# Performance work log

Hardware: AMD Instinct MI355X
Metric: run time of the kernel (lower is better)

Reference implementation:

```python
import jax, jax.numpy as jnp
import numpy as np

THETA = 10000.0

def apply_rope(x, positions):
    # x: [B, H, S, d_k], positions: [S] int
    d_k = x.shape[-1]
    inv_freq = THETA ** (-jnp.arange(0, d_k, 2, dtype=jnp.float32) / d_k)  # [d_k/2]
    ang = positions.astype(jnp.float32)[:, None] * inv_freq[None, :]        # [S, d_k/2]
    cos, sin = jnp.cos(ang), jnp.sin(ang)
    x_even = x[..., 0::2]
    x_odd = x[..., 1::2]
    r_even = x_even * cos - x_odd * sin
    r_odd = x_even * sin + x_odd * cos
    # interleave back
    return jnp.stack([r_even, r_odd], axis=-1).reshape(x.shape)

def setup_inputs() -> dict:
    key = jax.random.key(0)
    k1, k2, k3 = jax.random.split(key, 3)
    B, S, D = 2, 2048, 1024
    x = jax.random.normal(k1, (B, S, D), dtype=jnp.float32)
    token_positions = jnp.arange(S, dtype=jnp.int32)
    W_qkv = jax.random.normal(k2, (3 * D, D), dtype=jnp.float32) * 0.02
    W_o = jax.random.normal(k3, (D, D), dtype=jnp.float32) * 0.02
    return {"x": x, "token_positions": token_positions, "W_qkv": W_qkv, "W_o": W_o}

def reference(x, token_positions, W_qkv, W_o):
    B, S, D = x.shape
    H = 16
    d_k = D // H
    qkv = jnp.einsum('bsd,ed->bse', x, W_qkv)           # [B, S, 3D]
    q, k, v = jnp.split(qkv, 3, axis=-1)
    def to_heads(t):
        return t.reshape(B, S, H, d_k).transpose(0, 2, 1, 3)  # [B, H, S, d_k]
    hq, hk, hv = to_heads(q), to_heads(k), to_heads(v)
    hq = apply_rope(hq, token_positions)
    hk = apply_rope(hk, token_positions)
    scale = d_k ** -0.5
    scores = jnp.einsum('bhqd,bhkd->bhqk', hq, hk) * scale  # [B, H, S, S]
    causal = jnp.tril(jnp.ones((S, S), dtype=bool))
    scores = jnp.where(causal, scores, -jnp.inf)
    attn = jax.nn.softmax(scores, axis=-1)
    out = jnp.einsum('bhqk,bhkd->bhqd', attn, hv)           # [B, H, S, d_k]
    out = out.transpose(0, 2, 1, 3).reshape(B, S, D)
    return jnp.einsum('bsd,ed->bse', out, W_o)
```

## Files before the change

kernel.cpp:

```cpp
#include <hip/hip_runtime.h>
#include <math.h>

typedef short short8 __attribute__((ext_vector_type(8)));
typedef float f32x4 __attribute__((ext_vector_type(4)));

typedef __attribute__((address_space(1))) const void* as1p;
typedef __attribute__((address_space(3))) void* as3p;

__device__ __forceinline__ unsigned short f2bf(float f) {
    unsigned int u = __float_as_uint(f);
    u += 0x7fffu + ((u >> 16) & 1u);
    return (unsigned short)(u >> 16);
}
__device__ __forceinline__ float bf2f(unsigned int bits) {
    return __uint_as_float(bits << 16);
}

__global__ void cvt_all_bf16(const float* __restrict__ x,
                             const float* __restrict__ wqkv,
                             const float* __restrict__ wo,
                             unsigned short* __restrict__ xb,
                             unsigned short* __restrict__ wqkvb,
                             unsigned short* __restrict__ wob) {
    int i = blockIdx.x * blockDim.x + threadIdx.x;
    const float* src;
    unsigned short* dst;
    int off;
    if (i < 1048576)       { src = x;    dst = xb;    off = i; }
    else if (i < 1835008)  { src = wqkv; dst = wqkvb; off = i - 1048576; }
    else                   { src = wo;   dst = wob;   off = i - 1835008; }
    float4 v = ((const float4*)src)[off];
    ushort4 o = make_ushort4(f2bf(v.x), f2bf(v.y), f2bf(v.z), f2bf(v.w));
    ((ushort4*)dst)[off] = o;
}

template <int RF, int NTX, bool BF16_OUT, bool DO_ROPE>
__global__ __launch_bounds__(256) void gemm_nt_mfma(
    const unsigned short* __restrict__ A, const unsigned short* __restrict__ B,
    void* __restrict__ Cv, const int* __restrict__ pos, int N, int K) {
    constexpr int BM = RF * 32;
    __shared__ unsigned short As[BM * 32];
    __shared__ unsigned short Bs[128 * 32];
    const int tid = threadIdx.x;
    const int wave = tid >> 6, lane = tid & 63;
    const int L = blockIdx.x;
    const int xcd = L & 7, idx = L >> 3;
    const int nt_ = xcd * NTX + idx % NTX;
    const int mt  = idx / NTX;
    const int m0 = mt * BM, n0 = nt_ << 7;
    const int wr = ((wave >> 1) & 1) * (RF * 16);
    const int wc = (wave & 1) << 6;

    const int r0 = tid >> 2;
    const int ko = (((tid & 3) ^ ((r0 >> 1) & 3)) << 3);
    const unsigned short* Ap0 = A + (size_t)(m0 + r0) * K + ko;
    const unsigned short* Ap1 = A + (size_t)(m0 + (RF == 4 ? 64 : 0) + r0) * K + ko;
    const unsigned short* Bp0 = B + (size_t)(n0 + r0) * K + ko;
    const unsigned short* Bp1 = B + (size_t)(n0 + 64 + r0) * K + ko;

    f32x4 acc[RF][4] = {};
    const int lro = lane & 15;
    const int cs = ((lane >> 4) ^ ((lro >> 1) & 3)) << 3;

    for (int k0 = 0; k0 < K; k0 += 32) {
        __syncthreads();
        __builtin_amdgcn_global_load_lds((as1p)(Ap0 + k0), (as3p)(As + tid * 8), 16, 0, 0);
        if constexpr (RF == 4)
            __builtin_amdgcn_global_load_lds((as1p)(Ap1 + k0), (as3p)(As + (256 + tid) * 8), 16, 0, 0);
        __builtin_amdgcn_global_load_lds((as1p)(Bp0 + k0), (as3p)(Bs + tid * 8), 16, 0, 0);
        __builtin_amdgcn_global_load_lds((as1p)(Bp1 + k0), (as3p)(Bs + (256 + tid) * 8), 16, 0, 0);
        __syncthreads();

        short8 af[RF], bfr[4];
        #pragma unroll
        for (int i = 0; i < RF; i++) af[i] = *(const short8*)&As[(wr + i * 16 + lro) * 32 + cs];
        #pragma unroll
        for (int j = 0; j < 4; j++) bfr[j] = *(const short8*)&Bs[(wc + j * 16 + lro) * 32 + cs];
        #pragma unroll
        for (int i = 0; i < RF; i++)
            #pragma unroll
            for (int j = 0; j < 4; j++)
                acc[i][j] = __builtin_amdgcn_mfma_f32_16x16x32_bf16(af[i], bfr[j], acc[i][j], 0, 0, 0);
    }

    const int row_b = m0 + wr + ((lane >> 4) << 2);
    const int col_b = n0 + wc + lro;

    if constexpr (DO_ROPE) {
        const int sec = (n0 + wc) >> 10;
        if (sec < 2) {
            const float qs = (sec == 0) ? 0.18033688011112042f : 1.0f;
            const float sgn = (lane & 1) ? 1.0f : -1.0f;
            float ps[RF * 4];
            #pragma unroll
            for (int i = 0; i < RF; i++)
                #pragma unroll
                for (int r = 0; r < 4; r++)
                    ps[i * 4 + r] = (float)pos[(row_b + i * 16 + r) & 2047];
            #pragma unroll
            for (int j = 0; j < 4; j++) {
                float invf_rev = exp2f(-(float)((lro >> 1) + 8 * j) * 0.41524101186092029f)
                                 * 0.15915494309189535f;
                #pragma unroll
                for (int i = 0; i < RF; i++)
                    #pragma unroll
                    for (int r = 0; r < 4; r++) {
                        float rev = ps[i * 4 + r] * invf_rev;
                        rev -= floorf(rev);
                        float c = __builtin_amdgcn_cosf(rev) * qs;
                        float s = __builtin_amdgcn_sinf(rev) * (qs * sgn);
                        float mine = acc[i][j][r];
                        float partner = __shfl_xor(mine, 1, 64);
                        acc[i][j][r] = mine * c + partner * s;
                    }
            }
        }
    }

    #pragma unroll
    for (int i = 0; i < RF; i++)
        #pragma unroll
        for (int j = 0; j < 4; j++)
            #pragma unroll
            for (int r = 0; r < 4; r++) {
                size_t idx2 = (size_t)(row_b + i * 16 + r) * N + (col_b + j * 16);
                if constexpr (BF16_OUT) ((unsigned short*)Cv)[idx2] = f2bf(acc[i][j][r]);
                else ((float*)Cv)[idx2] = acc[i][j][r];
            }
}

__global__ __launch_bounds__(256) void flash_attn_mfma(
    const unsigned short* __restrict__ qkv, unsigned short* __restrict__ Ows) {
    const int S = 2048, D3 = 3072;
    const int L = blockIdx.x;
    const int xcd = L & 7, rr = L >> 3;
    const int qt = 31 - (rr >> 2);
    const int g2 = xcd + ((rr & 3) << 3);
    const int h = g2 & 15, b = g2 >> 4;
    const int tid = threadIdx.x, wave = tid >> 6, lane = tid & 63;
    const int lro = lane & 15, grp = lane >> 4;

    __shared__ __align__(16) unsigned short Ks[2][64 * 64];
    __shared__ __align__(16) unsigned int   Vp[2][64 * 36];
    __shared__ __align__(16) unsigned short Ps[64 * 80];

    const int sr = tid >> 3;
    const int sc = ((tid & 7) ^ (sr & 7)) << 3;
    const int kp = tid >> 3, vo = (tid & 7) << 3;
    const int vka = (kp >> 1) + ((kp & 1) << 5);
    const int vcol = (((kp >> 2) ^ (tid & 7)) << 2) | (kp & 3);

    const int cq = grp ^ (lro & 7);
    int kof0[4], kof1[4], vbse[4], vq[4];
    #pragma unroll
    for (int nt = 0; nt < 4; nt++) {
        int R = nt * 16 + lro;
        kof0[nt] = R * 64 + cq * 8;
        kof1[nt] = R * 64 + (cq ^ 4) * 8;
        vbse[nt] = R * 36;
        vq[nt] = (grp ^ (R >> 3)) << 2;
    }
    const int apo = (wave * 16 + lro) * 80 + grp * 8;
    const int prow = wave * 16 + grp * 4;

    const unsigned short* kbg = qkv + (size_t)(b * S) * D3 + 1024 + h * 64;
    const unsigned short* vbg = qkv + (size_t)(b * S) * D3 + 2048 + h * 64;

    const int q0 = qt << 6;
    const int nkt = qt + 1;

    const unsigned short* qrow =
        qkv + (size_t)(b * S + q0 + wave * 16 + lro) * D3 + h * 64 + grp * 8;
    short8 aq0 = *(const short8*)qrow;
    short8 aq1 = *(const short8*)(qrow + 32);

    __builtin_amdgcn_global_load_lds((as1p)(kbg + (size_t)sr * D3 + sc),
                                     (as3p)&Ks[0][tid * 8], 16, 0, 0);
    __builtin_amdgcn_global_load_lds((as1p)(kbg + (size_t)(sr + 32) * D3 + sc),
                                     (as3p)&Ks[0][(tid + 256) * 8], 16, 0, 0);
    {
        const unsigned short* vs = vbg + (size_t)vka * D3 + vo;
        uint4 va = *(const uint4*)vs;
        uint4 vb = *(const uint4*)(vs + (size_t)16 * D3);
        const unsigned short* pa = (const unsigned short*)&va;
        const unsigned short* pb = (const unsigned short*)&vb;
        #pragma unroll
        for (int j = 0; j < 8; j++)
            Vp[0][(vo + j) * 36 + vcol] = (unsigned)pa[j] | ((unsigned)pb[j] << 16);
    }
    __syncthreads();

    f32x4 acc_o[4] = {};
    float lsum[4] = {0.f, 0.f, 0.f, 0.f};

    for (int kt = 0; kt < nkt; kt++) {
        const int cur = kt & 1, nxt = cur ^ 1;
        const bool pf = (kt + 1 < nkt);
        uint4 va, vb;
        if (pf) {
            const unsigned short* kb1 = kbg + (size_t)((kt + 1) * 64) * D3;
            __builtin_amdgcn_global_load_lds((as1p)(kb1 + (size_t)sr * D3 + sc),
                                             (as3p)&Ks[nxt][tid * 8], 16, 0, 0);
            __builtin_amdgcn_global_load_lds((as1p)(kb1 + (size_t)(sr + 32) * D3 + sc),
                                             (as3p)&Ks[nxt][(tid + 256) * 8], 16, 0, 0);
            const unsigned short* vs = vbg + (size_t)((kt + 1) * 64 + vka) * D3 + vo;
            va = *(const uint4*)vs;
            vb = *(const uint4*)(vs + (size_t)16 * D3);
        }

        f32x4 s[4] = {};
        #pragma unroll
        for (int nt = 0; nt < 4; nt++) {
            short8 bk0 = *(const short8*)&Ks[cur][kof0[nt]];
            short8 bk1 = *(const short8*)&Ks[cur][kof1[nt]];
            s[nt] = __builtin_amdgcn_mfma_f32_16x16x32_bf16(aq0, bk0, s[nt], 0, 0, 0);
            s[nt] = __builtin_amdgcn_mfma_f32_16x16x32_bf16(aq1, bk1, s[nt], 0, 0, 0);
        }

        const bool diag = (kt == nkt - 1);
        #pragma unroll
        for (int r = 0; r < 4; r++) {
            float v0 = s[0][r], v1 = s[1][r], v2 = s[2][r], v3 = s[3][r];
            if (diag) {
                int rowl = prow + r;
                if (lro > rowl) v0 = -1e30f;
                if (16 + lro > rowl) v1 = -1e30f;
                if (32 + lro > rowl) v2 = -1e30f;
                if (48 + lro > rowl) v3 = -1e30f;
            }
            float p0 = __builtin_amdgcn_exp2f(v0);
            float p1 = __builtin_amdgcn_exp2f(v1);
            float p2 = __builtin_amdgcn_exp2f(v2);
            float p3 = __builtin_amdgcn_exp2f(v3);
            lsum[r] += (p0 + p1) + (p2 + p3);
            unsigned u0 = __float_as_uint(p0) + 0x8000u;
            unsigned u1 = __float_as_uint(p1) + 0x8000u;
            unsigned u2 = __float_as_uint(p2) + 0x8000u;
            unsigned u3 = __float_as_uint(p3) + 0x8000u;
            uint2 w = make_uint2((u0 >> 16) | (u1 & 0xffff0000u),
                                 (u2 >> 16) | (u3 & 0xffff0000u));
            *(uint2*)&Ps[(prow + r) * 80 + lro * 4] = w;
        }

        short8 ap0 = *(const short8*)&Ps[apo];
        short8 ap1 = *(const short8*)&Ps[apo + 32];
        #pragma unroll
        for (int nt = 0; nt < 4; nt++) {
            short8 bv0 = *(const short8*)&Vp[cur][vbse[nt] + vq[nt]];
            short8 bv1 = *(const short8*)&Vp[cur][vbse[nt] + (vq[nt] ^ 16)];
            acc_o[nt] = __builtin_amdgcn_mfma_f32_16x16x32_bf16(ap0, bv0, acc_o[nt], 0, 0, 0);
            acc_o[nt] = __builtin_amdgcn_mfma_f32_16x16x32_bf16(ap1, bv1, acc_o[nt], 0, 0, 0);
        }

        if (pf) {
            const unsigned short* pa = (const unsigned short*)&va;
            const unsigned short* pb = (const unsigned short*)&vb;
            #pragma unroll
            for (int j = 0; j < 8; j++)
                Vp[nxt][(vo + j) * 36 + vcol] = (unsigned)pa[j] | ((unsigned)pb[j] << 16);
        }
        __syncthreads();
    }

    #pragma unroll
    for (int r = 0; r < 4; r++) {
        float rsum = lsum[r];
        #pragma unroll
        for (int off = 1; off < 16; off <<= 1)
            rsum += __shfl_xor(rsum, off, 16);
        float inv = 1.0f / rsum;
        int row = q0 + prow + r;
        #pragma unroll
        for (int nt = 0; nt < 4; nt++)
            Ows[(size_t)(b * S + row) * 1024 + h * 64 + nt * 16 + lro] =
                f2bf(acc_o[nt][r] * inv);
    }
}

extern "C" void kernel_launch(void* const* d_in, const int* in_sizes, int n_in,
                              void* d_out, int out_size, void* d_ws, size_t ws_size,
                              hipStream_t stream) {
    const float* x    = (const float*)d_in[0];
    const int*   pos  = (const int*)d_in[1];
    const float* Wqkv = (const float*)d_in[2];
    const float* Wo   = (const float*)d_in[3];
    float* out = (float*)d_out;

    unsigned short* xb    = (unsigned short*)d_ws;
    unsigned short* Wqkvb = xb + (size_t)4096 * 1024;
    unsigned short* Wob   = Wqkvb + (size_t)3072 * 1024;
    unsigned short* qkvb  = Wob + (size_t)1024 * 1024;
    unsigned short* Owsb  = qkvb + (size_t)4096 * 3072;

    cvt_all_bf16<<<8192, 256, 0, stream>>>(x, Wqkv, Wo, xb, Wqkvb, Wob);

    gemm_nt_mfma<4, 3, true, true><<<768, 256, 0, stream>>>(
        xb, Wqkvb, qkvb, pos, 3072, 1024);

    flash_attn_mfma<<<1024, 256, 0, stream>>>(qkvb, Owsb);

    gemm_nt_mfma<2, 1, false, false><<<512, 256, 0, stream>>>(
        Owsb, Wob, out, nullptr, 1024, 1024);
}
```

Baseline: 189.4 us.

## Double flash-attention query tile to 128 rows per block for K/V reuse

Each block now processes 128 query rows, with each wave handling two 16-row fragments, so every K/V tile loaded into LDS feeds twice the MFMA work. The grid is halved and the block-to-(head, q-tile) mapping is reworked so the two halves of the grid pair long and short causal q-tiles for load balance. Causal masking now covers the last two 64-key tiles. In exchange, register pressure rises from the doubled accumulators, the P scratch buffer grows, and fewer blocks may leave some compute units idle.

```diff
diff --git a/kernel.cpp b/kernel.cpp
--- a/kernel.cpp
+++ b/kernel.cpp
@@ -133,16 +133,20 @@
     const unsigned short* __restrict__ qkv, unsigned short* __restrict__ Ows) {
     const int S = 2048, D3 = 3072;
     const int L = blockIdx.x;
-    const int xcd = L & 7, rr = L >> 3;
-    const int qt = 31 - (rr >> 2);
-    const int g2 = xcd + ((rr & 3) << 3);
+    const int xcd = L & 7;
+    const int rr  = (L >> 3) & 31;
+    const int kk  = L >> 8;
+    const int qt = kk ? (rr & 15) : (15 - (rr & 15));
+    const int g  = (kk << 1) + (rr >> 4);
+    const int g2 = xcd + (g << 3);
     const int h = g2 & 15, b = g2 >> 4;
     const int tid = threadIdx.x, wave = tid >> 6, lane = tid & 63;
     const int lro = lane & 15, grp = lane >> 4;
+    const int wb = wave << 5;
 
     __shared__ __align__(16) unsigned short Ks[2][64 * 64];
     __shared__ __align__(16) unsigned int   Vp[2][64 * 36];
-    __shared__ __align__(16) unsigned short Ps[64 * 80];
+    __shared__ __align__(16) unsigned short Ps[128 * 80];
 
     const int sr = tid >> 3;
     const int sc = ((tid & 7) ^ (sr & 7)) << 3;
@@ -160,19 +164,27 @@
         vbse[nt] = R * 36;
         vq[nt] = (grp ^ (R >> 3)) << 2;
     }
-    const int apo = (wave * 16 + lro) * 80 + grp * 8;
-    const int prow = wave * 16 + grp * 4;
+    int apo[2], prowv[2];
+    #pragma unroll
+    for (int rf = 0; rf < 2; rf++) {
+        apo[rf]   = (wb + rf * 16 + lro) * 80 + grp * 8;
+        prowv[rf] = wb + rf * 16 + grp * 4;
+    }
 
     const unsigned short* kbg = qkv + (size_t)(b * S) * D3 + 1024 + h * 64;
     const unsigned short* vbg = qkv + (size_t)(b * S) * D3 + 2048 + h * 64;
 
-    const int q0 = qt << 6;
-    const int nkt = qt + 1;
-
-    const unsigned short* qrow =
-        qkv + (size_t)(b * S + q0 + wave * 16 + lro) * D3 + h * 64 + grp * 8;
-    short8 aq0 = *(const short8*)qrow;
-    short8 aq1 = *(const short8*)(qrow + 32);
+    const int q0 = qt << 7;
+    const int nkt = 2 * qt + 2;
+
+    short8 aq[2][2];
+    #pragma unroll
+    for (int rf = 0; rf < 2; rf++) {
+        const unsigned short* qrow =
+            qkv + (size_t)(b * S + q0 + wb + rf * 16 + lro) * D3 + h * 64 + grp * 8;
+        aq[rf][0] = *(const short8*)qrow;
+        aq[rf][1] = *(const short8*)(qrow + 32);
+    }
 
     __builtin_amdgcn_global_load_lds((as1p)(kbg + (size_t)sr * D3 + sc),
                                      (as3p)&Ks[0][tid * 8], 16, 0, 0);
@@ -190,8 +202,8 @@
     }
     __syncthreads();
 
-    f32x4 acc_o[4] = {};
-    float lsum[4] = {0.f, 0.f, 0.f, 0.f};
+    f32x4 acc_o[2][4] = {};
+    float lsum[2][4] = {};
 
     for (int kt = 0; kt < nkt; kt++) {
         const int cur = kt & 1, nxt = cur ^ 1;
@@ -208,48 +220,62 @@
             vb = *(const uint4*)(vs + (size_t)16 * D3);
         }
 
-        f32x4 s[4] = {};
+        f32x4 s[2][4] = {};
         #pragma unroll
         for (int nt = 0; nt < 4; nt++) {
             short8 bk0 = *(const short8*)&Ks[cur][kof0[nt]];
             short8 bk1 = *(const short8*)&Ks[cur][kof1[nt]];
-            s[nt] = __builtin_amdgcn_mfma_f32_16x16x32_bf16(aq0, bk0, s[nt], 0, 0, 0);
-            s[nt] = __builtin_amdgcn_mfma_f32_16x16x32_bf16(aq1, bk1, s[nt], 0, 0, 0);
-        }
-
-        const bool diag = (kt == nkt - 1);
-        #pragma unroll
-        for (int r = 0; r < 4; r++) {
-            float v0 = s[0][r], v1 = s[1][r], v2 = s[2][r], v3 = s[3][r];
-            if (diag) {
-                int rowl = prow + r;
-                if (lro > rowl) v0 = -1e30f;
-                if (16 + lro > rowl) v1 = -1e30f;
-                if (32 + lro > rowl) v2 = -1e30f;
-                if (48 + lro > rowl) v3 = -1e30f;
-            }
-            float p0 = __builtin_amdgcn_exp2f(v0);
-            float p1 = __builtin_amdgcn_exp2f(v1);
-            float p2 = __builtin_amdgcn_exp2f(v2);
-            float p3 = __builtin_amdgcn_exp2f(v3);
-            lsum[r] += (p0 + p1) + (p2 + p3);
-            unsigned u0 = __float_as_uint(p0) + 0x8000u;
-            unsigned u1 = __float_as_uint(p1) + 0x8000u;
-            unsigned u2 = __float_as_uint(p2) + 0x8000u;
-            unsigned u3 = __float_as_uint(p3) + 0x8000u;
-            uint2 w = make_uint2((u0 >> 16) | (u1 & 0xffff0000u),
-                                 (u2 >> 16) | (u3 & 0xffff0000u));
-            *(uint2*)&Ps[(prow + r) * 80 + lro * 4] = w;
-        }
-
-        short8 ap0 = *(const short8*)&Ps[apo];
-        short8 ap1 = *(const short8*)&Ps[apo + 32];
+            #pragma unroll
+            for (int rf = 0; rf < 2; rf++) {
+                s[rf][nt] = __builtin_amdgcn_mfma_f32_16x16x32_bf16(aq[rf][0], bk0, s[rf][nt], 0, 0, 0);
+                s[rf][nt] = __builtin_amdgcn_mfma_f32_16x16x32_bf16(aq[rf][1], bk1, s[rf][nt], 0, 0, 0);
+            }
+        }
+
+        const bool dg = (kt >= nkt - 2);
+        const int moff = dg ? ((kt - (nkt - 2)) << 6) : 0;
+        #pragma unroll
+        for (int rf = 0; rf < 2; rf++) {
+            #pragma unroll
+            for (int r = 0; r < 4; r++) {
+                float v0 = s[rf][0][r], v1 = s[rf][1][r], v2 = s[rf][2][r], v3 = s[rf][3][r];
+                if (dg) {
+                    int thr = prowv[rf] + r - moff;
+                    if (lro > thr) v0 = -1e30f;
+                    if (16 + lro > thr) v1 = -1e30f;
+                    if (32 + lro > thr) v2 = -1e30f;
+                    if (48 + lro > thr) v3 = -1e30f;
+                }
+                float p0 = __builtin_amdgcn_exp2f(v0);
+                float p1 = __builtin_amdgcn_exp2f(v1);
+                float p2 = __builtin_amdgcn_exp2f(v2);
+                float p3 = __builtin_amdgcn_exp2f(v3);
+                lsum[rf][r] += (p0 + p1) + (p2 + p3);
+                unsigned u0 = __float_as_uint(p0) + 0x8000u;
+                unsigned u1 = __float_as_uint(p1) + 0x8000u;
+                unsigned u2 = __float_as_uint(p2) + 0x8000u;
+                unsigned u3 = __float_as_uint(p3) + 0x8000u;
+                uint2 w = make_uint2((u0 >> 16) | (u1 & 0xffff0000u),
+                                     (u2 >> 16) | (u3 & 0xffff0000u));
+                *(uint2*)&Ps[(prowv[rf] + r) * 80 + lro * 4] = w;
+            }
+        }
+
+        short8 ap[2][2];
+        #pragma unroll
+        for (int rf = 0; rf < 2; rf++) {
+            ap[rf][0] = *(const short8*)&Ps[apo[rf]];
+            ap[rf][1] = *(const short8*)&Ps[apo[rf] + 32];
+        }
         #pragma unroll
         for (int nt = 0; nt < 4; nt++) {
             short8 bv0 = *(const short8*)&Vp[cur][vbse[nt] + vq[nt]];
             short8 bv1 = *(const short8*)&Vp[cur][vbse[nt] + (vq[nt] ^ 16)];
-            acc_o[nt] = __builtin_amdgcn_mfma_f32_16x16x32_bf16(ap0, bv0, acc_o[nt], 0, 0, 0);
-            acc_o[nt] = __builtin_amdgcn_mfma_f32_16x16x32_bf16(ap1, bv1, acc_o[nt], 0, 0, 0);
+            #pragma unroll
+            for (int rf = 0; rf < 2; rf++) {
+                acc_o[rf][nt] = __builtin_amdgcn_mfma_f32_16x16x32_bf16(ap[rf][0], bv0, acc_o[rf][nt], 0, 0, 0);
+                acc_o[rf][nt] = __builtin_amdgcn_mfma_f32_16x16x32_bf16(ap[rf][1], bv1, acc_o[rf][nt], 0, 0, 0);
+            }
         }
 
         if (pf) {
@@ -263,17 +289,20 @@
     }
 
     #pragma unroll
-    for (int r = 0; r < 4; r++) {
-        float rsum = lsum[r];
-        #pragma unroll
-        for (int off = 1; off < 16; off <<= 1)
-            rsum += __shfl_xor(rsum, off, 16);
-        float inv = 1.0f / rsum;
-        int row = q0 + prow + r;
-        #pragma unroll
-        for (int nt = 0; nt < 4; nt++)
-            Ows[(size_t)(b * S + row) * 1024 + h * 64 + nt * 16 + lro] =
-                f2bf(acc_o[nt][r] * inv);
+    for (int rf = 0; rf < 2; rf++) {
+        #pragma unroll
+        for (int r = 0; r < 4; r++) {
+            float rsum = lsum[rf][r];
+            #pragma unroll
+            for (int off = 1; off < 16; off <<= 1)
+                rsum += __shfl_xor(rsum, off, 16);
+            float inv = 1.0f / rsum;
+            int row = q0 + prowv[rf] + r;
+            #pragma unroll
+            for (int nt = 0; nt < 4; nt++)
+                Ows[(size_t)(b * S + row) * 1024 + h * 64 + nt * 16 + lro] =
+                    f2bf(acc_o[rf][nt][r] * inv);
+        }
     }
 }
 
@@ -297,7 +326,7 @@
     gemm_nt_mfma<4, 3, true, true><<<768, 256, 0, stream>>>(
         xb, Wqkvb, qkvb, pos, 3072, 1024);
 
-    flash_attn_mfma<<<1024, 256, 0, stream>>>(qkvb, Owsb);
+    flash_attn_mfma<<<512, 256, 0, stream>>>(qkvb, Owsb);
 
     gemm_nt_mfma<2, 1, false, false><<<512, 256, 0, stream>>>(
         Owsb, Wob, out, nullptr, 1024, 1024);
```

After: 194.3 us. +2.6%, slower.
